# Performance work log

Hardware: AMD Instinct MI355X
Metric: run time of the kernel (lower is better)

Reference implementation:

```python
import jax, jax.numpy as jnp
import numpy as np

BLOCK = 32          # MX spec: 32-element blocks share one E8M0 scale
E4M3_MAX = 448.0    # max finite value of float8_e4m3fn
EMAX_E4M3 = 8       # exponent of largest e4m3 binade (448 = 1.75 * 2^8)
MIN_NORM_EXP = -6   # smallest normal exponent of e4m3 (subnormals below)
MANT_BITS = 3


def _round_e4m3(v):
    """Emulate round-to-nearest cast to float8_e4m3fn (saturating)."""
    a = jnp.abs(v)
    # exponent of each element, clamped so subnormals use the -6 binade step
    e = jnp.clip(jnp.floor(jnp.log2(jnp.maximum(a, 1e-30))), MIN_NORM_EXP, EMAX_E4M3)
    step = jnp.exp2(e - MANT_BITS)          # quantization step in this binade
    q = jnp.round(a / step) * step
    q = jnp.minimum(q, E4M3_MAX)            # saturate (e4m3fn has no inf)
    return jnp.sign(v) * q


def quantize_mx_dequant(x):
    """MX quantize a 2D [M, K] tensor with E8M0 per-32-block scales to e4m3,
    then dequantize (q * scale). Math-equivalent to the xq/x_scales pair fed
    into torch._scaled_mm."""
    M, K = x.shape
    xb = x.reshape(M, K // BLOCK, BLOCK)
    amax = jnp.max(jnp.abs(xb), axis=-1, keepdims=True)
    # E8M0 shared scale: 2^(floor(log2(amax)) - emax_elem), clamped to E8M0 range
    exp = jnp.floor(jnp.log2(jnp.maximum(amax, 1e-30))) - EMAX_E4M3
    exp = jnp.clip(exp, -127.0, 127.0)
    scale = jnp.exp2(exp)
    q = _round_e4m3(xb / scale)
    return (q * scale).reshape(M, K)


def setup_inputs() -> dict:
    key = jax.random.key(0)
    k1, k2, k3 = jax.random.split(key, 3)
    x = jax.random.normal(k1, (8192, 4096), dtype=jnp.float32)
    weight = jax.random.normal(k2, (4096, 4096), dtype=jnp.float32) * 0.02
    bias = jax.random.normal(k3, (4096,), dtype=jnp.float32) * 0.02
    return {"x": x, "weight": weight, "bias": bias}


def reference(x, weight, bias):
    x_2d = x.reshape(-1, x.shape[-1])            # [M, K]
    xd = quantize_mx_dequant(x_2d)               # MX-quantized activations
    wd = quantize_mx_dequant(weight)             # MX-quantized weights (buffer wq/w_scales)
    out = xd @ wd.T + bias                       # scaled matmul + bias
    return out.reshape(*x.shape[:-1], out.shape[-1])
```

## Files before the change

### kernel.cpp

```cpp
#include <hip/hip_runtime.h>

typedef __attribute__((ext_vector_type(8))) short bf16x8;
typedef __attribute__((ext_vector_type(4))) float f32x4;
typedef __attribute__((ext_vector_type(4))) unsigned short u16x4;

#define BM 256
#define BN 256
#define BK 64

__device__ __forceinline__ float pow2i(int e) {
  if (e >= -126) return __uint_as_float((unsigned)(e + 127) << 23);
  return __uint_as_float(0x00400000u >> (-126 - e));
}

__device__ __forceinline__ float qdq_e4m3(float x, float inv, float scale) {
  float s = x * inv;
  float a = fabsf(s);
  int ee = (int)((__float_as_uint(a) >> 23) & 0xffu) - 127;
  ee = ee < -6 ? -6 : (ee > 8 ? 8 : ee);
  float istep = __uint_as_float((unsigned)(130 - ee) << 23);
  float step  = __uint_as_float((unsigned)(124 + ee) << 23);
  float q = rintf(a * istep) * step;
  q = fminf(q, 448.0f);
  return copysignf(q, s) * scale;
}

__global__ void quant_mx(const float4* __restrict__ in, u16x4* __restrict__ outq,
                         long long n4) {
  long long idx = (long long)blockIdx.x * blockDim.x + threadIdx.x;
  long long stride = (long long)gridDim.x * blockDim.x;
  for (; idx < n4; idx += stride) {
    float4 v = in[idx];
    float am = fmaxf(fmaxf(fabsf(v.x), fabsf(v.y)), fmaxf(fabsf(v.z), fabsf(v.w)));
    am = fmaxf(am, __shfl_xor(am, 1));
    am = fmaxf(am, __shfl_xor(am, 2));
    am = fmaxf(am, __shfl_xor(am, 4));
    int e = (int)((__float_as_uint(am) >> 23) & 0xffu) - 135;
    e = e < -127 ? -127 : (e > 127 ? 127 : e);
    float scale = pow2i(e);
    float inv   = pow2i(-e);
    float r0 = qdq_e4m3(v.x, inv, scale);
    float r1 = qdq_e4m3(v.y, inv, scale);
    float r2 = qdq_e4m3(v.z, inv, scale);
    float r3 = qdq_e4m3(v.w, inv, scale);
    u16x4 o;
    o[0] = (unsigned short)(__float_as_uint(r0) >> 16);
    o[1] = (unsigned short)(__float_as_uint(r1) >> 16);
    o[2] = (unsigned short)(__float_as_uint(r2) >> 16);
    o[3] = (unsigned short)(__float_as_uint(r3) >> 16);
    outq[idx] = o;
  }
}

__device__ __forceinline__ void gload_lds16(const void* g, void* l) {
  __builtin_amdgcn_global_load_lds(
      (const __attribute__((address_space(1))) unsigned int*)g,
      (__attribute__((address_space(3))) unsigned int*)l, 16, 0, 0);
}

#define BAR() do { asm volatile("" ::: "memory"); \
                   __builtin_amdgcn_s_barrier();  \
                   asm volatile("" ::: "memory"); } while (0)

__global__ __launch_bounds__(512, 2) void gemm_mx(
    const unsigned short* __restrict__ A, const unsigned short* __restrict__ B,
    const float* __restrict__ bias, float* __restrict__ C,
    int M, int N, int K) {
  __shared__ __align__(16) unsigned short As[2][BM * BK];
  __shared__ __align__(16) unsigned short Bs[2][BN * BK];

  const int tid = threadIdx.x;
  const int l  = tid & 63, w = tid >> 6;
  const int wr = w >> 2, wc = w & 3;
  const int rr = l & 15, kq = l >> 4;

  const int nbx = N / BN;
  const int bid = blockIdx.x;
  const int cpx = gridDim.x >> 3;
  const int swz = (bid & 7) * cpx + (bid >> 3);
  const int by = swz / nbx, bx = swz % nbx;

  const unsigned short* gA = A + (size_t)by * BM * K;
  const unsigned short* gB = B + (size_t)bx * BN * K;

  f32x4 acc[8][4] = {};

  const int swx   = (rr & 7) * 8;
  const int kofs0 = (kq * 8) ^ swx;
  const int kofs1 = (32 + kq * 8) ^ swx;

#define STAGE(G, L, CH, KT) do {                                   \
    int _ch = (CH);                                                \
    int _row = _ch >> 3;                                           \
    int _c16 = (_ch & 7) ^ (_row & 7);                             \
    gload_lds16((G) + (size_t)_row * K + (KT) + _c16 * 8,          \
                (L) + _ch * 8);                                    \
  } while (0)

  bf16x8 af[4][2], bg[2][2];

#define READ_A(MH) _Pragma("unroll")                               \
  for (int m = 0; m < 4; ++m) {                                    \
    const int rb = (wr * 128 + ((MH) * 4 + m) * 16 + rr) * BK;     \
    af[m][0] = *(const bf16x8*)&Ac[rb + kofs0];                    \
    af[m][1] = *(const bf16x8*)&Ac[rb + kofs1];                    \
  }
#define READ_B(NH) _Pragma("unroll")                               \
  for (int n = 0; n < 2; ++n) {                                    \
    const int rb = (wc * 64 + ((NH) * 2 + n) * 16 + rr) * BK;      \
    bg[n][0] = *(const bf16x8*)&Bc[rb + kofs0];                    \
    bg[n][1] = *(const bf16x8*)&Bc[rb + kofs1];                    \
  }
#define MFMA16(MH, NH)                                             \
  asm volatile("s_waitcnt lgkmcnt(0)" ::: "memory");               \
  __builtin_amdgcn_s_setprio(1);                                   \
  _Pragma("unroll")                                                \
  for (int kk = 0; kk < 2; ++kk)                                   \
    _Pragma("unroll")                                              \
    for (int m = 0; m < 4; ++m)                                    \
      _Pragma("unroll")                                            \
      for (int n = 0; n < 2; ++n)                                  \
        acc[(MH)*4+m][(NH)*2+n] = __builtin_amdgcn_mfma_f32_16x16x32_bf16( \
            af[m][kk], bg[n][kk], acc[(MH)*4+m][(NH)*2+n], 0, 0, 0);\
  __builtin_amdgcn_s_setprio(0);

  {
    unsigned short* Ad = As[0];
    unsigned short* Bd = Bs[0];
    STAGE(gA, Ad, tid,        0); STAGE(gA, Ad, tid + 512,  0);
    STAGE(gA, Ad, tid + 1024, 0); STAGE(gA, Ad, tid + 1536, 0);
    STAGE(gB, Bd, tid,        0); STAGE(gB, Bd, tid + 512,  0);
    STAGE(gB, Bd, tid + 1024, 0); STAGE(gB, Bd, tid + 1536, 0);
  }

  const int NTK = K / BK;
  int cur = 0;
  for (int t = 0; t < NTK; ++t) {
    const bool pf = (t + 1 < NTK);
    const int ktn = (t + 1) * BK;
    unsigned short* Ac = As[cur];
    unsigned short* Bc = Bs[cur];
    unsigned short* An = As[cur ^ 1];
    unsigned short* Bn = Bs[cur ^ 1];

    if (pf) {
      STAGE(gA, An, tid, ktn); STAGE(gA, An, tid + 512, ktn);
      asm volatile("s_waitcnt vmcnt(2)" ::: "memory");
    } else {
      asm volatile("s_waitcnt vmcnt(0)" ::: "memory");
    }
    BAR();
    READ_A(0) READ_B(0)
    MFMA16(0, 0)
    BAR();

    READ_B(1)
    if (pf) { STAGE(gA, An, tid + 1024, ktn); STAGE(gA, An, tid + 1536, ktn); }
    BAR();
    MFMA16(0, 1)
    BAR();

    READ_A(1) READ_B(0)
    if (pf) { STAGE(gB, Bn, tid, ktn); STAGE(gB, Bn, tid + 512, ktn); }
    BAR();
    MFMA16(1, 0)
    BAR();

    READ_B(1)
    if (pf) { STAGE(gB, Bn, tid + 1024, ktn); STAGE(gB, Bn, tid + 1536, ktn); }
    BAR();
    MFMA16(1, 1)
    BAR();

    cur ^= 1;
  }

#pragma unroll
  for (int ni = 0; ni < 4; ++ni) {
    const int col = bx * BN + wc * 64 + ni * 16 + rr;
    const float bv = bias[col];
#pragma unroll
    for (int mi = 0; mi < 8; ++mi) {
      const int row0 = by * BM + wr * 128 + mi * 16 + kq * 4;
#pragma unroll
      for (int j = 0; j < 4; ++j) {
        C[(size_t)(row0 + j) * N + col] = acc[mi][ni][j] + bv;
      }
    }
  }
}

extern "C" void kernel_launch(void* const* d_in, const int* in_sizes, int n_in,
                              void* d_out, int out_size, void* d_ws, size_t ws_size,
                              hipStream_t stream) {
  const float* x    = (const float*)d_in[0];
  const float* wt   = (const float*)d_in[1];
  const float* bias = (const float*)d_in[2];
  float* out = (float*)d_out;

  const int N = in_sizes[2];
  const int K = (int)((long long)in_sizes[1] / N);
  const int M = (int)((long long)in_sizes[0] / K);

  unsigned short* xq = (unsigned short*)d_ws;
  unsigned short* wq = xq + (size_t)M * K;

  long long nx4 = (long long)M * K / 4;
  long long nw4 = (long long)N * K / 4;
  quant_mx<<<2048, 256, 0, stream>>>((const float4*)x,  (u16x4*)xq, nx4);
  quant_mx<<<2048, 256, 0, stream>>>((const float4*)wt, (u16x4*)wq, nw4);

  dim3 grid((M / BM) * (N / BN));
  gemm_mx<<<grid, 512, 0, stream>>>(xq, wq, bias, out, M, N, K);
}
```

Measured before the change: 613.9 us.

## Restructure GEMM K-loop prefetch schedule and batch quantize loads per thread

The GEMM main loop now issues all A prefetches in the first phase and all B prefetches in the second. It keeps B fragments for both N halves in registers so the last two MFMA phases need no extra B reads, and waits for global loads only once at the end of each K step. Separately, the quantize kernel gives each thread four float4 elements, loading them all before computing, with the grid sized to match. This aims to raise memory-level parallelism and cut barrier stalls, at the cost of extra VGPRs that could cause spills under the 2-wave launch bound.

```diff
diff --git a/kernel.cpp b/kernel.cpp
--- a/kernel.cpp
+++ b/kernel.cpp
@@ -25,31 +25,42 @@
   return copysignf(q, s) * scale;
 }
 
+__device__ __forceinline__ u16x4 qdq_pack(float4 v) {
+  float am = fmaxf(fmaxf(fabsf(v.x), fabsf(v.y)), fmaxf(fabsf(v.z), fabsf(v.w)));
+  am = fmaxf(am, __shfl_xor(am, 1));
+  am = fmaxf(am, __shfl_xor(am, 2));
+  am = fmaxf(am, __shfl_xor(am, 4));
+  int e = (int)((__float_as_uint(am) >> 23) & 0xffu) - 135;
+  e = e < -127 ? -127 : (e > 127 ? 127 : e);
+  float scale = pow2i(e);
+  float inv   = pow2i(-e);
+  u16x4 o;
+  o[0] = (unsigned short)(__float_as_uint(qdq_e4m3(v.x, inv, scale)) >> 16);
+  o[1] = (unsigned short)(__float_as_uint(qdq_e4m3(v.y, inv, scale)) >> 16);
+  o[2] = (unsigned short)(__float_as_uint(qdq_e4m3(v.z, inv, scale)) >> 16);
+  o[3] = (unsigned short)(__float_as_uint(qdq_e4m3(v.w, inv, scale)) >> 16);
+  return o;
+}
+
 __global__ void quant_mx(const float4* __restrict__ in, u16x4* __restrict__ outq,
                          long long n4) {
-  long long idx = (long long)blockIdx.x * blockDim.x + threadIdx.x;
-  long long stride = (long long)gridDim.x * blockDim.x;
-  for (; idx < n4; idx += stride) {
-    float4 v = in[idx];
-    float am = fmaxf(fmaxf(fabsf(v.x), fabsf(v.y)), fmaxf(fabsf(v.z), fabsf(v.w)));
-    am = fmaxf(am, __shfl_xor(am, 1));
-    am = fmaxf(am, __shfl_xor(am, 2));
-    am = fmaxf(am, __shfl_xor(am, 4));
-    int e = (int)((__float_as_uint(am) >> 23) & 0xffu) - 135;
-    e = e < -127 ? -127 : (e > 127 ? 127 : e);
-    float scale = pow2i(e);
-    float inv   = pow2i(-e);
-    float r0 = qdq_e4m3(v.x, inv, scale);
-    float r1 = qdq_e4m3(v.y, inv, scale);
-    float r2 = qdq_e4m3(v.z, inv, scale);
-    float r3 = qdq_e4m3(v.w, inv, scale);
-    u16x4 o;
-    o[0] = (unsigned short)(__float_as_uint(r0) >> 16);
-    o[1] = (unsigned short)(__float_as_uint(r1) >> 16);
-    o[2] = (unsigned short)(__float_as_uint(r2) >> 16);
-    o[3] = (unsigned short)(__float_as_uint(r3) >> 16);
-    outq[idx] = o;
-  }
+  const long long base = (long long)blockIdx.x * blockDim.x + threadIdx.x;
+  const long long stride = (long long)gridDim.x * blockDim.x;
+  const long long i0 = base, i1 = base + stride, i2 = base + 2 * stride, i3 = base + 3 * stride;
+  float4 v0, v1, v2, v3;
+  if (i0 < n4) v0 = in[i0];
+  if (i1 < n4) v1 = in[i1];
+  if (i2 < n4) v2 = in[i2];
+  if (i3 < n4) v3 = in[i3];
+  u16x4 o0, o1, o2, o3;
+  if (i0 < n4) o0 = qdq_pack(v0);
+  if (i1 < n4) o1 = qdq_pack(v1);
+  if (i2 < n4) o2 = qdq_pack(v2);
+  if (i3 < n4) o3 = qdq_pack(v3);
+  if (i0 < n4) outq[i0] = o0;
+  if (i1 < n4) outq[i1] = o1;
+  if (i2 < n4) outq[i2] = o2;
+  if (i3 < n4) outq[i3] = o3;
 }
 
 __device__ __forceinline__ void gload_lds16(const void* g, void* l) {
@@ -61,6 +72,8 @@
 #define BAR() do { asm volatile("" ::: "memory"); \
                    __builtin_amdgcn_s_barrier();  \
                    asm volatile("" ::: "memory"); } while (0)
+#define WAIT_LGKM() asm volatile("s_waitcnt lgkmcnt(0)" ::: "memory")
+#define WAIT_VM0()  asm volatile("s_waitcnt vmcnt(0)" ::: "memory")
 
 __global__ __launch_bounds__(512, 2) void gemm_mx(
     const unsigned short* __restrict__ A, const unsigned short* __restrict__ B,
@@ -97,7 +110,7 @@
                 (L) + _ch * 8);                                    \
   } while (0)
 
-  bf16x8 af[4][2], bg[2][2];
+  bf16x8 af[4][2], bg[4][2];
 
 #define READ_A(MH) _Pragma("unroll")                               \
   for (int m = 0; m < 4; ++m) {                                    \
@@ -108,11 +121,10 @@
 #define READ_B(NH) _Pragma("unroll")                               \
   for (int n = 0; n < 2; ++n) {                                    \
     const int rb = (wc * 64 + ((NH) * 2 + n) * 16 + rr) * BK;      \
-    bg[n][0] = *(const bf16x8*)&Bc[rb + kofs0];                    \
-    bg[n][1] = *(const bf16x8*)&Bc[rb + kofs1];                    \
+    bg[(NH) * 2 + n][0] = *(const bf16x8*)&Bc[rb + kofs0];         \
+    bg[(NH) * 2 + n][1] = *(const bf16x8*)&Bc[rb + kofs1];         \
   }
 #define MFMA16(MH, NH)                                             \
-  asm volatile("s_waitcnt lgkmcnt(0)" ::: "memory");               \
   __builtin_amdgcn_s_setprio(1);                                   \
   _Pragma("unroll")                                                \
   for (int kk = 0; kk < 2; ++kk)                                   \
@@ -121,7 +133,7 @@
       _Pragma("unroll")                                            \
       for (int n = 0; n < 2; ++n)                                  \
         acc[(MH)*4+m][(NH)*2+n] = __builtin_amdgcn_mfma_f32_16x16x32_bf16( \
-            af[m][kk], bg[n][kk], acc[(MH)*4+m][(NH)*2+n], 0, 0, 0);\
+            af[m][kk], bg[(NH)*2+n][kk], acc[(MH)*4+m][(NH)*2+n], 0, 0, 0);\
   __builtin_amdgcn_s_setprio(0);
 
   {
@@ -131,6 +143,8 @@
     STAGE(gA, Ad, tid + 1024, 0); STAGE(gA, Ad, tid + 1536, 0);
     STAGE(gB, Bd, tid,        0); STAGE(gB, Bd, tid + 512,  0);
     STAGE(gB, Bd, tid + 1024, 0); STAGE(gB, Bd, tid + 1536, 0);
+    WAIT_VM0();
+    BAR();
   }
 
   const int NTK = K / BK;
@@ -143,33 +157,34 @@
     unsigned short* An = As[cur ^ 1];
     unsigned short* Bn = Bs[cur ^ 1];
 
+    READ_A(0) READ_B(0)
     if (pf) {
-      STAGE(gA, An, tid, ktn); STAGE(gA, An, tid + 512, ktn);
-      asm volatile("s_waitcnt vmcnt(2)" ::: "memory");
-    } else {
-      asm volatile("s_waitcnt vmcnt(0)" ::: "memory");
+      STAGE(gA, An, tid,        ktn); STAGE(gA, An, tid + 512,  ktn);
+      STAGE(gA, An, tid + 1024, ktn); STAGE(gA, An, tid + 1536, ktn);
     }
     BAR();
-    READ_A(0) READ_B(0)
+    WAIT_LGKM();
     MFMA16(0, 0)
     BAR();
 
     READ_B(1)
-    if (pf) { STAGE(gA, An, tid + 1024, ktn); STAGE(gA, An, tid + 1536, ktn); }
-    BAR();
+    if (pf) {
+      STAGE(gB, Bn, tid,        ktn); STAGE(gB, Bn, tid + 512,  ktn);
+      STAGE(gB, Bn, tid + 1024, ktn); STAGE(gB, Bn, tid + 1536, ktn);
+    }
+    BAR();
+    WAIT_LGKM();
     MFMA16(0, 1)
     BAR();
 
-    READ_A(1) READ_B(0)
-    if (pf) { STAGE(gB, Bn, tid, ktn); STAGE(gB, Bn, tid + 512, ktn); }
-    BAR();
+    READ_A(1)
+    BAR();
+    WAIT_LGKM();
+    MFMA16(1, 1)
+    BAR();
+
     MFMA16(1, 0)
-    BAR();
-
-    READ_B(1)
-    if (pf) { STAGE(gB, Bn, tid + 1024, ktn); STAGE(gB, Bn, tid + 1536, ktn); }
-    BAR();
-    MFMA16(1, 1)
+    WAIT_VM0();
     BAR();
 
     cur ^= 1;
@@ -207,8 +222,10 @@
 
   long long nx4 = (long long)M * K / 4;
   long long nw4 = (long long)N * K / 4;
-  quant_mx<<<2048, 256, 0, stream>>>((const float4*)x,  (u16x4*)xq, nx4);
-  quant_mx<<<2048, 256, 0, stream>>>((const float4*)wt, (u16x4*)wq, nw4);
+  int gx = (int)((nx4 + 4LL * 256 - 1) / (4LL * 256));
+  int gw = (int)((nw4 + 4LL * 256 - 1) / (4LL * 256));
+  quant_mx<<<gx, 256, 0, stream>>>((const float4*)x,  (u16x4*)xq, nx4);
+  quant_mx<<<gw, 256, 0, stream>>>((const float4*)wt, (u16x4*)wq, nw4);
 
   dim3 grid((M / BM) * (N / BN));
   gemm_mx<<<grid, 512, 0, stream>>>(xq, wq, bias, out, M, N, K);
```

New measurement: 529.4 us. 13.8% less time.
